# Optimization experiments

Measured on AMD Instinct MI355X. Metric: run time of the kernel, lower is better.

Reference implementation:

```python
import jax, jax.numpy as jnp
import numpy as np

N_NODES = 100000
N_EDGES = 3200000
D_FEAT = 512
D_HID = 64
N_CLS = 40


def setup_inputs() -> dict:
    key = jax.random.key(0)
    k1, k2, k3, k4, k5, k6, k7 = jax.random.split(key, 7)
    x = jax.random.normal(k1, (N_NODES, D_FEAT), dtype=jnp.float32)
    edge_index = jax.random.randint(k2, (2, N_EDGES), 0, N_NODES, dtype=jnp.int64)
    edge_weight = jax.random.uniform(k3, (N_EDGES,), dtype=jnp.float32)
    # GCNConv params (glorot-ish scale)
    W1 = jax.random.normal(k4, (D_FEAT, D_HID), dtype=jnp.float32) / np.sqrt(D_FEAT)
    b1 = jnp.zeros((D_HID,), dtype=jnp.float32)
    W2 = jax.random.normal(k5, (D_HID, N_CLS), dtype=jnp.float32) / np.sqrt(D_HID)
    b2 = jnp.zeros((N_CLS,), dtype=jnp.float32)
    return {"x": x, "edge_index": edge_index, "edge_weight": edge_weight,
            "W1": W1, "b1": b1, "W2": W2, "b2": b2}


def _gcn_norm(edge_index, edge_weight, num_nodes):
    # add self-loops with weight 1 (PyG gcn_norm default)
    loop = jnp.arange(num_nodes, dtype=edge_index.dtype)
    row = jnp.concatenate([edge_index[0], loop])
    col = jnp.concatenate([edge_index[1], loop])
    ew = jnp.concatenate([edge_weight, jnp.ones((num_nodes,), edge_weight.dtype)])
    deg = jax.ops.segment_sum(ew, col, num_segments=num_nodes)  # in-degree (weighted)
    dinv = jnp.where(deg > 0, jax.lax.rsqrt(deg), 0.0)
    norm = dinv[row] * ew * dinv[col]
    return row, col, norm


def _gcn_conv(x, row, col, norm, W, b, num_nodes):
    x = x @ W  # linear first (out_channels small): [N, out]
    msg = norm[:, None] * x[row]            # gather + scale: [E+N, out]
    out = jax.ops.segment_sum(msg, col, num_segments=num_nodes)  # scatter-add
    return out + b


def reference(x, edge_index, edge_weight, W1, b1, W2, b2):
    n = x.shape[0]
    row, col, norm = _gcn_norm(edge_index, edge_weight, n)
    h = jax.nn.relu(_gcn_conv(x, row, col, norm, W1, b1, n))
    # dropout omitted (eval-mode determinism for correctness baseline)
    logits = _gcn_conv(h, row, col, norm, W2, b2, n)
    return jax.nn.log_softmax(logits, axis=1)
```

## Files before the change

kernel.cpp:

```cpp
#include <hip/hip_runtime.h>
#include <math.h>

#define N_NODES 100000
#define N_EDGES 3200000
#define D_FEAT  512
#define D_HID   64
#define N_CLS   40
#define NBKT    391
#define NBLKA   256
#define EPB     (N_EDGES / NBLKA)

typedef __attribute__((ext_vector_type(8))) short short8;
typedef __attribute__((ext_vector_type(4))) float floatx4;

static __device__ __forceinline__ unsigned short f2bf(float f) {
    unsigned u = __float_as_uint(f);
    unsigned r = (u + 0x7FFFu + ((u >> 16) & 1u)) >> 16;
    return (unsigned short)r;
}
static __device__ __forceinline__ float bf2f(unsigned short h) {
    return __uint_as_float(((unsigned)h) << 16);
}
static __device__ __forceinline__ short8 pack_bf16x8(float4 a, float4 b) {
    short8 r;
    r[0] = (short)f2bf(a.x); r[1] = (short)f2bf(a.y);
    r[2] = (short)f2bf(a.z); r[3] = (short)f2bf(a.w);
    r[4] = (short)f2bf(b.x); r[5] = (short)f2bf(b.y);
    r[6] = (short)f2bf(b.z); r[7] = (short)f2bf(b.w);
    return r;
}


__global__ __launch_bounds__(256) void k_histA(const int* __restrict__ ei,
                                               int* __restrict__ mat) {
    __shared__ int hist[NBKT];
    const int tid = threadIdx.x, blk = blockIdx.x;
    for (int i = tid; i < NBKT; i += 256) hist[i] = 0;
    __syncthreads();
    const int e0 = blk * EPB, e1 = e0 + EPB;
    for (int e = e0 + tid; e < e1; e += 256)
        atomicAdd(&hist[ei[N_EDGES + e] >> 8], 1);
    __syncthreads();
    for (int i = tid; i < NBKT; i += 256) mat[i * NBLKA + blk] = hist[i];
}


__global__ __launch_bounds__(256) void k_scanRows(int* __restrict__ mat,
                                                  int* __restrict__ total) {
    __shared__ int s[256];
    const int tid = threadIdx.x, bin = blockIdx.x;
    int v = mat[bin * NBLKA + tid];
    s[tid] = v;
    __syncthreads();
    for (int off = 1; off < 256; off <<= 1) {
        int t = (tid >= off) ? s[tid - off] : 0;
        __syncthreads();
        s[tid] += t;
        __syncthreads();
    }
    mat[bin * NBLKA + tid] = s[tid] - v;
    if (tid == 255) total[bin] = s[255];
}


__global__ __launch_bounds__(512) void k_scanTot(const int* __restrict__ total,
                                                 int* __restrict__ cbase) {
    __shared__ int s[512];
    const int tid = threadIdx.x;
    int v = (tid < NBKT) ? total[tid] : 0;
    s[tid] = v;
    __syncthreads();
    for (int off = 1; off < 512; off <<= 1) {
        int t = (tid >= off) ? s[tid - off] : 0;
        __syncthreads();
        s[tid] += t;
        __syncthreads();
    }
    if (tid <= NBKT) cbase[tid] = s[tid] - v;
}


__global__ __launch_bounds__(256) void k_scatterB(const int* __restrict__ ei,
                                                  const float* __restrict__ ew,
                                                  const int* __restrict__ mat,
                                                  const int* __restrict__ cbase,
                                                  int2* __restrict__ tmpA,
                                                  unsigned char* __restrict__ tmpD) {
    __shared__ int cur[NBKT];
    const int tid = threadIdx.x, blk = blockIdx.x;
    for (int i = tid; i < NBKT; i += 256)
        cur[i] = cbase[i] + mat[i * NBLKA + blk];
    __syncthreads();
    const int e0 = blk * EPB, e1 = e0 + EPB;
    for (int e = e0 + tid; e < e1; e += 256) {
        int r = ei[e];
        int c = ei[N_EDGES + e];
        int slot = atomicAdd(&cur[c >> 8], 1);
        tmpA[slot] = make_int2(r, __float_as_int(ew[e]));
        tmpD[slot] = (unsigned char)(c & 255);
    }
}


__global__ __launch_bounds__(256) void k_bucketC(const int* __restrict__ cbase,
                                                 const int2* __restrict__ tmpA,
                                                 const unsigned char* __restrict__ tmpD,
                                                 int2* __restrict__ csr,
                                                 int* __restrict__ cnt,
                                                 int* __restrict__ base,
                                                 float* __restrict__ dinv) {
    __shared__ int   c_cnt[256];
    __shared__ float c_deg[256];
    __shared__ int   c_scan[256];
    __shared__ int   c_cur[256];
    const int tid = threadIdx.x, b = blockIdx.x;
    const int s = cbase[b], e = cbase[b + 1];
    c_cnt[tid] = 0;
    c_deg[tid] = 0.f;
    __syncthreads();
    for (int j = s + tid; j < e; j += 256) {
        int d = tmpD[j];
        atomicAdd(&c_cnt[d], 1);
        atomicAdd(&c_deg[d], __int_as_float(tmpA[j].y));
    }
    __syncthreads();
    int v = c_cnt[tid];
    c_scan[tid] = v;
    __syncthreads();
    for (int off = 1; off < 256; off <<= 1) {
        int t = (tid >= off) ? c_scan[tid - off] : 0;
        __syncthreads();
        c_scan[tid] += t;
        __syncthreads();
    }
    int excl = c_scan[tid] - v;
    c_cur[tid] = excl;
    int node = b * 256 + tid;
    if (node < N_NODES) {
        cnt[node]  = v;
        base[node] = s + excl;
        dinv[node] = rsqrtf(1.0f + c_deg[tid]);
    }
    __syncthreads();
    for (int j = s + tid; j < e; j += 256) {
        int d = tmpD[j];
        int slot = atomicAdd(&c_cur[d], 1);
        csr[s + slot] = tmpA[j];
    }
}


__global__ __launch_bounds__(256) void k_gemm1(const float* __restrict__ x,
                                               const float* __restrict__ W1,
                                               unsigned short* __restrict__ hpre) {
    __shared__ __align__(16) short Wt[64 * 512];
    const int tid = threadIdx.x;

    {
        const int c  = tid & 63;
        const int kb = (tid >> 6) * 128;
        const int sw = (c & 7) << 3;
        for (int kk = 0; kk < 128; kk += 8) {
            short8 v;
#pragma unroll
            for (int j = 0; j < 8; j++)
                v[j] = (short)f2bf(W1[(size_t)(kb + kk + j) * D_HID + c]);
            *(short8*)&Wt[c * 512 + ((kb + kk) ^ sw)] = v;
        }
    }
    __syncthreads();

    const int widx = blockIdx.x * 4 + (tid >> 6);
    if (widx >= N_NODES / 16) return;
    const int lane = tid & 63;
    const int q  = lane >> 4;
    const int cn = lane & 15;
    const int r0 = widx * 16;
    const int sw = (cn & 7) << 3;

    floatx4 acc[4] = {{0,0,0,0},{0,0,0,0},{0,0,0,0},{0,0,0,0}};
    const float* xp = x + (size_t)(r0 + cn) * D_FEAT + q * 8;

#pragma unroll 4
    for (int k0 = 0; k0 < D_FEAT; k0 += 32) {
        float4 xa = *(const float4*)(xp + k0);
        float4 xb = *(const float4*)(xp + k0 + 4);
        short8 a = pack_bf16x8(xa, xb);
#pragma unroll
        for (int ct = 0; ct < 4; ct++) {
            short8 b = *(const short8*)&Wt[(ct * 16 + cn) * 512 + ((k0 + q * 8) ^ sw)];
            acc[ct] = __builtin_amdgcn_mfma_f32_16x16x32_bf16(a, b, acc[ct], 0, 0, 0);
        }
    }

#pragma unroll
    for (int ct = 0; ct < 4; ct++)
#pragma unroll
        for (int i = 0; i < 4; i++)
            hpre[(size_t)(r0 + q * 4 + i) * D_HID + ct * 16 + cn] = f2bf(acc[ct][i]);
}


__global__ __launch_bounds__(256) void k_gather1(const int* __restrict__ base,
                                                 const int* __restrict__ cnt,
                                                 const int2* __restrict__ csr,
                                                 const unsigned short* __restrict__ hpre,
                                                 const float* __restrict__ dinv,
                                                 const float* __restrict__ b1,
                                                 const float* __restrict__ W2,
                                                 float* __restrict__ z) {
    __shared__ float hs[4][64];
    int lane = threadIdx.x & 63;
    int w = threadIdx.x >> 6;
    int n = blockIdx.x * 4 + w;
    int s = base[n], e = s + cnt[n];
    float dn = dinv[n];
    float a0 = dn * bf2f(hpre[(size_t)n * D_HID + lane]);
    float a1 = 0.f, a2 = 0.f, a3 = 0.f, a4 = 0.f, a5 = 0.f, a6 = 0.f, a7 = 0.f;
    int j = s;
    for (; j + 7 < e; j += 8) {
        int2 p0 = csr[j];     int2 p1 = csr[j + 1];
        int2 p2 = csr[j + 2]; int2 p3 = csr[j + 3];
        int2 p4 = csr[j + 4]; int2 p5 = csr[j + 5];
        int2 p6 = csr[j + 6]; int2 p7 = csr[j + 7];
        float w0 = dinv[p0.x] * __int_as_float(p0.y);
        float w1 = dinv[p1.x] * __int_as_float(p1.y);
        float w2 = dinv[p2.x] * __int_as_float(p2.y);
        float w3 = dinv[p3.x] * __int_as_float(p3.y);
        float w4 = dinv[p4.x] * __int_as_float(p4.y);
        float w5 = dinv[p5.x] * __int_as_float(p5.y);
        float w6 = dinv[p6.x] * __int_as_float(p6.y);
        float w7 = dinv[p7.x] * __int_as_float(p7.y);
        a0 += w0 * bf2f(hpre[(size_t)p0.x * D_HID + lane]);
        a1 += w1 * bf2f(hpre[(size_t)p1.x * D_HID + lane]);
        a2 += w2 * bf2f(hpre[(size_t)p2.x * D_HID + lane]);
        a3 += w3 * bf2f(hpre[(size_t)p3.x * D_HID + lane]);
        a4 += w4 * bf2f(hpre[(size_t)p4.x * D_HID + lane]);
        a5 += w5 * bf2f(hpre[(size_t)p5.x * D_HID + lane]);
        a6 += w6 * bf2f(hpre[(size_t)p6.x * D_HID + lane]);
        a7 += w7 * bf2f(hpre[(size_t)p7.x * D_HID + lane]);
    }
    for (; j + 3 < e; j += 4) {
        int2 p0 = csr[j];     int2 p1 = csr[j + 1];
        int2 p2 = csr[j + 2]; int2 p3 = csr[j + 3];
        float w0 = dinv[p0.x] * __int_as_float(p0.y);
        float w1 = dinv[p1.x] * __int_as_float(p1.y);
        float w2 = dinv[p2.x] * __int_as_float(p2.y);
        float w3 = dinv[p3.x] * __int_as_float(p3.y);
        a0 += w0 * bf2f(hpre[(size_t)p0.x * D_HID + lane]);
        a1 += w1 * bf2f(hpre[(size_t)p1.x * D_HID + lane]);
        a2 += w2 * bf2f(hpre[(size_t)p2.x * D_HID + lane]);
        a3 += w3 * bf2f(hpre[(size_t)p3.x * D_HID + lane]);
    }
    for (; j < e; j++) {
        int2 p = csr[j];
        a0 += dinv[p.x] * __int_as_float(p.y) * bf2f(hpre[(size_t)p.x * D_HID + lane]);
    }
    float h = dn * (((a0 + a1) + (a2 + a3)) + ((a4 + a5) + (a6 + a7))) + b1[lane];
    h = h > 0.f ? h : 0.f;
    hs[w][lane] = h;
    __syncthreads();
    if (lane < N_CLS) {
        float acc = 0.f;
#pragma unroll 8
        for (int k = 0; k < D_HID; k++)
            acc += hs[w][k] * W2[k * N_CLS + lane];
        z[(size_t)n * N_CLS + lane] = acc;
    }
}


__global__ __launch_bounds__(256) void k_gather2_lsm(const int* __restrict__ base,
                                                     const int* __restrict__ cnt,
                                                     const int2* __restrict__ csr,
                                                     const float* __restrict__ z,
                                                     const float* __restrict__ dinv,
                                                     const float* __restrict__ b2,
                                                     float* __restrict__ out) {
    int lane = threadIdx.x & 63;
    int n = blockIdx.x * 4 + (threadIdx.x >> 6);
    bool act = lane < N_CLS;
    int fl = act ? lane : (N_CLS - 1);
    int s = base[n], e = s + cnt[n];
    float dn = dinv[n];
    float a0 = dn * z[(size_t)n * N_CLS + fl];
    float a1 = 0.f, a2 = 0.f, a3 = 0.f, a4 = 0.f, a5 = 0.f, a6 = 0.f, a7 = 0.f;
    int j = s;
    for (; j + 7 < e; j += 8) {
        int2 p0 = csr[j];     int2 p1 = csr[j + 1];
        int2 p2 = csr[j + 2]; int2 p3 = csr[j + 3];
        int2 p4 = csr[j + 4]; int2 p5 = csr[j + 5];
        int2 p6 = csr[j + 6]; int2 p7 = csr[j + 7];
        float w0 = dinv[p0.x] * __int_as_float(p0.y);
        float w1 = dinv[p1.x] * __int_as_float(p1.y);
        float w2 = dinv[p2.x] * __int_as_float(p2.y);
        float w3 = dinv[p3.x] * __int_as_float(p3.y);
        float w4 = dinv[p4.x] * __int_as_float(p4.y);
        float w5 = dinv[p5.x] * __int_as_float(p5.y);
        float w6 = dinv[p6.x] * __int_as_float(p6.y);
        float w7 = dinv[p7.x] * __int_as_float(p7.y);
        a0 += w0 * z[(size_t)p0.x * N_CLS + fl];
        a1 += w1 * z[(size_t)p1.x * N_CLS + fl];
        a2 += w2 * z[(size_t)p2.x * N_CLS + fl];
        a3 += w3 * z[(size_t)p3.x * N_CLS + fl];
        a4 += w4 * z[(size_t)p4.x * N_CLS + fl];
        a5 += w5 * z[(size_t)p5.x * N_CLS + fl];
        a6 += w6 * z[(size_t)p6.x * N_CLS + fl];
        a7 += w7 * z[(size_t)p7.x * N_CLS + fl];
    }
    for (; j + 3 < e; j += 4) {
        int2 p0 = csr[j];     int2 p1 = csr[j + 1];
        int2 p2 = csr[j + 2]; int2 p3 = csr[j + 3];
        float w0 = dinv[p0.x] * __int_as_float(p0.y);
        float w1 = dinv[p1.x] * __int_as_float(p1.y);
        float w2 = dinv[p2.x] * __int_as_float(p2.y);
        float w3 = dinv[p3.x] * __int_as_float(p3.y);
        a0 += w0 * z[(size_t)p0.x * N_CLS + fl];
        a1 += w1 * z[(size_t)p1.x * N_CLS + fl];
        a2 += w2 * z[(size_t)p2.x * N_CLS + fl];
        a3 += w3 * z[(size_t)p3.x * N_CLS + fl];
    }
    for (; j < e; j++) {
        int2 p = csr[j];
        a0 += dinv[p.x] * __int_as_float(p.y) * z[(size_t)p.x * N_CLS + fl];
    }
    float logit = dn * (((a0 + a1) + (a2 + a3)) + ((a4 + a5) + (a6 + a7))) + b2[fl];
    float m = act ? logit : -INFINITY;
    for (int off = 32; off; off >>= 1) m = fmaxf(m, __shfl_xor(m, off, 64));
    float ev = act ? expf(logit - m) : 0.f;
    float sum = ev;
    for (int off = 32; off; off >>= 1) sum += __shfl_xor(sum, off, 64);
    if (act) out[(size_t)n * N_CLS + lane] = logit - m - logf(sum);
}


extern "C" void kernel_launch(void* const* d_in, const int* in_sizes, int n_in,
                              void* d_out, int out_size, void* d_ws, size_t ws_size,
                              hipStream_t stream) {
    const float* x  = (const float*)d_in[0];
    const int*   ei = (const int*)d_in[1];
    const float* ew = (const float*)d_in[2];
    const float* W1 = (const float*)d_in[3];
    const float* b1 = (const float*)d_in[4];
    const float* W2 = (const float*)d_in[5];
    const float* b2 = (const float*)d_in[6];
    float* out = (float*)d_out;

    int* ws = (int*)d_ws;
    int2*          csr  = (int2*)ws;
    int2*          tmpA = (int2*)(ws + 2 * (size_t)N_EDGES);
    unsigned char* tmpD = (unsigned char*)(ws + 4 * (size_t)N_EDGES);
    int*   mat   = ws + 4 * (size_t)N_EDGES + N_EDGES / 4;
    int*   total = mat + NBKT * NBLKA;
    int*   cbase = total + NBKT;
    int*   cnt   = cbase + NBKT + 1;
    int*   base  = cnt + N_NODES;
    float* dinv  = (float*)(base + N_NODES);
    unsigned short* hpre = (unsigned short*)tmpA;
    float* z = (float*)(hpre + (size_t)N_NODES * D_HID);

    k_histA   <<<NBLKA, 256, 0, stream>>>(ei, mat);
    k_scanRows<<<NBKT,  256, 0, stream>>>(mat, total);
    k_scanTot <<<1,     512, 0, stream>>>(total, cbase);
    k_scatterB<<<NBLKA, 256, 0, stream>>>(ei, ew, mat, cbase, tmpA, tmpD);
    k_bucketC <<<NBKT,  256, 0, stream>>>(cbase, tmpA, tmpD, csr, cnt, base, dinv);
    k_gemm1   <<<(N_NODES / 16 + 3) / 4, 256, 0, stream>>>(x, W1, hpre);
    k_gather1 <<<N_NODES / 4, 256, 0, stream>>>(base, cnt, csr, hpre, dinv, b1, W2, z);
    k_gather2_lsm<<<N_NODES / 4, 256, 0, stream>>>(base, cnt, csr, z, dinv, b2, out);
}
```

Baseline: 798.0 us.

## Precompute edge norms into CSR and broadcast edges via readlane in gathers

Folds the full GCN normalization, dinv[row]*ew*dinv[col], into the CSR edge weights. The destination factor is applied in k_bucketC and the source factor in a new k_norm pass, so the gather kernels no longer do a random dinv lookup per edge. The gathers now load 64 edges cooperatively, one per lane, and broadcast each with readlane. They accumulate into 16 independent registers to expose more memory-level parallelism. Also pads z rows to 48 floats, relocates the workspace buffers, and drops a __syncthreads in gather1, relying on intra-wave lockstep for the shared hs buffer. The new k_norm launch adds a full extra pass over the CSR array.

```diff
diff --git a/kernel.cpp b/kernel.cpp
--- a/kernel.cpp
+++ b/kernel.cpp
@@ -6,6 +6,7 @@
 #define D_FEAT  512
 #define D_HID   64
 #define N_CLS   40
+#define ZSTR    48
 #define NBKT    391
 #define NBLKA   256
 #define EPB     (N_EDGES / NBLKA)
@@ -113,6 +114,7 @@
     __shared__ float c_deg[256];
     __shared__ int   c_scan[256];
     __shared__ int   c_cur[256];
+    __shared__ float c_dnv[256];
     const int tid = threadIdx.x, b = blockIdx.x;
     const int s = cbase[b], e = cbase[b + 1];
     c_cnt[tid] = 0;
@@ -135,18 +137,30 @@
     }
     int excl = c_scan[tid] - v;
     c_cur[tid] = excl;
+    float dv = rsqrtf(1.0f + c_deg[tid]);
+    c_dnv[tid] = dv;
     int node = b * 256 + tid;
     if (node < N_NODES) {
         cnt[node]  = v;
         base[node] = s + excl;
-        dinv[node] = rsqrtf(1.0f + c_deg[tid]);
+        dinv[node] = dv;
     }
     __syncthreads();
     for (int j = s + tid; j < e; j += 256) {
         int d = tmpD[j];
+        int2 p = tmpA[j];
         int slot = atomicAdd(&c_cur[d], 1);
-        csr[s + slot] = tmpA[j];
-    }
+        csr[s + slot] = make_int2(p.x, __float_as_int(__int_as_float(p.y) * c_dnv[d]));
+    }
+}
+
+
+__global__ __launch_bounds__(256) void k_norm(int2* __restrict__ csr,
+                                              const float* __restrict__ dinv) {
+    int i = blockIdx.x * 256 + threadIdx.x;
+    int2 p = csr[i];
+    p.y = __float_as_int(__int_as_float(p.y) * dinv[p.x]);
+    csr[i] = p;
 }
 
 
@@ -210,62 +224,45 @@
                                                  const float* __restrict__ W2,
                                                  float* __restrict__ z) {
     __shared__ float hs[4][64];
-    int lane = threadIdx.x & 63;
-    int w = threadIdx.x >> 6;
-    int n = blockIdx.x * 4 + w;
-    int s = base[n], e = s + cnt[n];
-    float dn = dinv[n];
-    float a0 = dn * bf2f(hpre[(size_t)n * D_HID + lane]);
-    float a1 = 0.f, a2 = 0.f, a3 = 0.f, a4 = 0.f, a5 = 0.f, a6 = 0.f, a7 = 0.f;
-    int j = s;
-    for (; j + 7 < e; j += 8) {
-        int2 p0 = csr[j];     int2 p1 = csr[j + 1];
-        int2 p2 = csr[j + 2]; int2 p3 = csr[j + 3];
-        int2 p4 = csr[j + 4]; int2 p5 = csr[j + 5];
-        int2 p6 = csr[j + 6]; int2 p7 = csr[j + 7];
-        float w0 = dinv[p0.x] * __int_as_float(p0.y);
-        float w1 = dinv[p1.x] * __int_as_float(p1.y);
-        float w2 = dinv[p2.x] * __int_as_float(p2.y);
-        float w3 = dinv[p3.x] * __int_as_float(p3.y);
-        float w4 = dinv[p4.x] * __int_as_float(p4.y);
-        float w5 = dinv[p5.x] * __int_as_float(p5.y);
-        float w6 = dinv[p6.x] * __int_as_float(p6.y);
-        float w7 = dinv[p7.x] * __int_as_float(p7.y);
-        a0 += w0 * bf2f(hpre[(size_t)p0.x * D_HID + lane]);
-        a1 += w1 * bf2f(hpre[(size_t)p1.x * D_HID + lane]);
-        a2 += w2 * bf2f(hpre[(size_t)p2.x * D_HID + lane]);
-        a3 += w3 * bf2f(hpre[(size_t)p3.x * D_HID + lane]);
-        a4 += w4 * bf2f(hpre[(size_t)p4.x * D_HID + lane]);
-        a5 += w5 * bf2f(hpre[(size_t)p5.x * D_HID + lane]);
-        a6 += w6 * bf2f(hpre[(size_t)p6.x * D_HID + lane]);
-        a7 += w7 * bf2f(hpre[(size_t)p7.x * D_HID + lane]);
-    }
-    for (; j + 3 < e; j += 4) {
-        int2 p0 = csr[j];     int2 p1 = csr[j + 1];
-        int2 p2 = csr[j + 2]; int2 p3 = csr[j + 3];
-        float w0 = dinv[p0.x] * __int_as_float(p0.y);
-        float w1 = dinv[p1.x] * __int_as_float(p1.y);
-        float w2 = dinv[p2.x] * __int_as_float(p2.y);
-        float w3 = dinv[p3.x] * __int_as_float(p3.y);
-        a0 += w0 * bf2f(hpre[(size_t)p0.x * D_HID + lane]);
-        a1 += w1 * bf2f(hpre[(size_t)p1.x * D_HID + lane]);
-        a2 += w2 * bf2f(hpre[(size_t)p2.x * D_HID + lane]);
-        a3 += w3 * bf2f(hpre[(size_t)p3.x * D_HID + lane]);
-    }
-    for (; j < e; j++) {
-        int2 p = csr[j];
-        a0 += dinv[p.x] * __int_as_float(p.y) * bf2f(hpre[(size_t)p.x * D_HID + lane]);
-    }
-    float h = dn * (((a0 + a1) + (a2 + a3)) + ((a4 + a5) + (a6 + a7))) + b1[lane];
+    const int lane = threadIdx.x & 63;
+    const int w = threadIdx.x >> 6;
+    const int n = blockIdx.x * 4 + w;
+    const int s = base[n], e = s + cnt[n];
+    const float dn = dinv[n];
+
+    float acc[16];
+#pragma unroll
+    for (int u = 0; u < 16; u++) acc[u] = 0.f;
+    acc[0] = dn * dn * bf2f(hpre[(size_t)n * D_HID + lane]);
+
+    for (int c = s; c < e; c += 64) {
+        int idx = c + lane;
+        int idxc = idx < e ? idx : (e - 1);
+        int2 ed = csr[idxc];
+        if (idx >= e) ed.y = 0;
+        int nc = e - c; if (nc > 64) nc = 64;
+        for (int j = 0; j < nc; j += 16) {
+#pragma unroll
+            for (int u = 0; u < 16; u++) {
+                int   src = __builtin_amdgcn_readlane(ed.x, j + u);
+                float wj  = __uint_as_float((unsigned)__builtin_amdgcn_readlane(ed.y, j + u));
+                const unsigned short* rp = hpre + ((size_t)src << 6);
+                acc[u] = fmaf(wj, bf2f(rp[lane]), acc[u]);
+            }
+        }
+    }
+
+    float h = ((acc[0] + acc[1]) + (acc[2] + acc[3])) + ((acc[4] + acc[5]) + (acc[6] + acc[7]))
+            + ((acc[8] + acc[9]) + (acc[10] + acc[11])) + ((acc[12] + acc[13]) + (acc[14] + acc[15]));
+    h += b1[lane];
     h = h > 0.f ? h : 0.f;
     hs[w][lane] = h;
-    __syncthreads();
     if (lane < N_CLS) {
-        float acc = 0.f;
+        float a2 = 0.f;
 #pragma unroll 8
         for (int k = 0; k < D_HID; k++)
-            acc += hs[w][k] * W2[k * N_CLS + lane];
-        z[(size_t)n * N_CLS + lane] = acc;
+            a2 += hs[w][k] * W2[k * N_CLS + lane];
+        z[(size_t)n * ZSTR + lane] = a2;
     }
 }
 
@@ -277,54 +274,38 @@
                                                      const float* __restrict__ dinv,
                                                      const float* __restrict__ b2,
                                                      float* __restrict__ out) {
-    int lane = threadIdx.x & 63;
-    int n = blockIdx.x * 4 + (threadIdx.x >> 6);
-    bool act = lane < N_CLS;
-    int fl = act ? lane : (N_CLS - 1);
-    int s = base[n], e = s + cnt[n];
-    float dn = dinv[n];
-    float a0 = dn * z[(size_t)n * N_CLS + fl];
-    float a1 = 0.f, a2 = 0.f, a3 = 0.f, a4 = 0.f, a5 = 0.f, a6 = 0.f, a7 = 0.f;
-    int j = s;
-    for (; j + 7 < e; j += 8) {
-        int2 p0 = csr[j];     int2 p1 = csr[j + 1];
-        int2 p2 = csr[j + 2]; int2 p3 = csr[j + 3];
-        int2 p4 = csr[j + 4]; int2 p5 = csr[j + 5];
-        int2 p6 = csr[j + 6]; int2 p7 = csr[j + 7];
-        float w0 = dinv[p0.x] * __int_as_float(p0.y);
-        float w1 = dinv[p1.x] * __int_as_float(p1.y);
-        float w2 = dinv[p2.x] * __int_as_float(p2.y);
-        float w3 = dinv[p3.x] * __int_as_float(p3.y);
-        float w4 = dinv[p4.x] * __int_as_float(p4.y);
-        float w5 = dinv[p5.x] * __int_as_float(p5.y);
-        float w6 = dinv[p6.x] * __int_as_float(p6.y);
-        float w7 = dinv[p7.x] * __int_as_float(p7.y);
-        a0 += w0 * z[(size_t)p0.x * N_CLS + fl];
-        a1 += w1 * z[(size_t)p1.x * N_CLS + fl];
-        a2 += w2 * z[(size_t)p2.x * N_CLS + fl];
-        a3 += w3 * z[(size_t)p3.x * N_CLS + fl];
-        a4 += w4 * z[(size_t)p4.x * N_CLS + fl];
-        a5 += w5 * z[(size_t)p5.x * N_CLS + fl];
-        a6 += w6 * z[(size_t)p6.x * N_CLS + fl];
-        a7 += w7 * z[(size_t)p7.x * N_CLS + fl];
-    }
-    for (; j + 3 < e; j += 4) {
-        int2 p0 = csr[j];     int2 p1 = csr[j + 1];
-        int2 p2 = csr[j + 2]; int2 p3 = csr[j + 3];
-        float w0 = dinv[p0.x] * __int_as_float(p0.y);
-        float w1 = dinv[p1.x] * __int_as_float(p1.y);
-        float w2 = dinv[p2.x] * __int_as_float(p2.y);
-        float w3 = dinv[p3.x] * __int_as_float(p3.y);
-        a0 += w0 * z[(size_t)p0.x * N_CLS + fl];
-        a1 += w1 * z[(size_t)p1.x * N_CLS + fl];
-        a2 += w2 * z[(size_t)p2.x * N_CLS + fl];
-        a3 += w3 * z[(size_t)p3.x * N_CLS + fl];
-    }
-    for (; j < e; j++) {
-        int2 p = csr[j];
-        a0 += dinv[p.x] * __int_as_float(p.y) * z[(size_t)p.x * N_CLS + fl];
-    }
-    float logit = dn * (((a0 + a1) + (a2 + a3)) + ((a4 + a5) + (a6 + a7))) + b2[fl];
+    const int lane = threadIdx.x & 63;
+    const int n = blockIdx.x * 4 + (threadIdx.x >> 6);
+    const bool act = lane < N_CLS;
+    const int fl = act ? lane : (N_CLS - 1);
+    const int s = base[n], e = s + cnt[n];
+    const float dn = dinv[n];
+
+    float acc[16];
+#pragma unroll
+    for (int u = 0; u < 16; u++) acc[u] = 0.f;
+    acc[0] = dn * dn * z[(size_t)n * ZSTR + fl];
+
+    for (int c = s; c < e; c += 64) {
+        int idx = c + lane;
+        int idxc = idx < e ? idx : (e - 1);
+        int2 ed = csr[idxc];
+        if (idx >= e) ed.y = 0;
+        int nc = e - c; if (nc > 64) nc = 64;
+        for (int j = 0; j < nc; j += 16) {
+#pragma unroll
+            for (int u = 0; u < 16; u++) {
+                int   src = __builtin_amdgcn_readlane(ed.x, j + u);
+                float wj  = __uint_as_float((unsigned)__builtin_amdgcn_readlane(ed.y, j + u));
+                const float* rp = z + (size_t)src * ZSTR;
+                acc[u] = fmaf(wj, rp[fl], acc[u]);
+            }
+        }
+    }
+
+    float logit = ((acc[0] + acc[1]) + (acc[2] + acc[3])) + ((acc[4] + acc[5]) + (acc[6] + acc[7]))
+                + ((acc[8] + acc[9]) + (acc[10] + acc[11])) + ((acc[12] + acc[13]) + (acc[14] + acc[15]));
+    logit += b2[fl];
     float m = act ? logit : -INFINITY;
     for (int off = 32; off; off >>= 1) m = fmaxf(m, __shfl_xor(m, off, 64));
     float ev = act ? expf(logit - m) : 0.f;
@@ -353,17 +334,18 @@
     int*   mat   = ws + 4 * (size_t)N_EDGES + N_EDGES / 4;
     int*   total = mat + NBKT * NBLKA;
     int*   cbase = total + NBKT;
-    int*   cnt   = cbase + NBKT + 1;
-    int*   base  = cnt + N_NODES;
-    float* dinv  = (float*)(base + N_NODES);
     unsigned short* hpre = (unsigned short*)tmpA;
-    float* z = (float*)(hpre + (size_t)N_NODES * D_HID);
+    float* z = (float*)(ws + 2 * (size_t)N_EDGES + (size_t)N_NODES * D_HID / 2);
+    int*   cnt  = ws + 2 * (size_t)N_EDGES + (size_t)N_NODES * D_HID / 2 + (size_t)N_NODES * ZSTR;
+    int*   base = cnt + N_NODES;
+    float* dinv = (float*)(base + N_NODES);
 
     k_histA   <<<NBLKA, 256, 0, stream>>>(ei, mat);
     k_scanRows<<<NBKT,  256, 0, stream>>>(mat, total);
     k_scanTot <<<1,     512, 0, stream>>>(total, cbase);
     k_scatterB<<<NBLKA, 256, 0, stream>>>(ei, ew, mat, cbase, tmpA, tmpD);
     k_bucketC <<<NBKT,  256, 0, stream>>>(cbase, tmpA, tmpD, csr, cnt, base, dinv);
+    k_norm    <<<N_EDGES / 256, 256, 0, stream>>>(csr, dinv);
     k_gemm1   <<<(N_NODES / 16 + 3) / 4, 256, 0, stream>>>(x, W1, hpre);
     k_gather1 <<<N_NODES / 4, 256, 0, stream>>>(base, cnt, csr, hpre, dinv, b1, W2, z);
     k_gather2_lsm<<<N_NODES / 4, 256, 0, stream>>>(base, cnt, csr, z, dinv, b2, out);
```

New measurement: 727.0 us. 1.1x faster.
